# Kernel tuning notes

Hardware: AMD Instinct MI355X
Metric: run time of the kernel (lower is better)

## Reference

```python
import jax, jax.numpy as jnp
import numpy as np

B, N, K = 4, 16384, 8
NF = [8, 32, 64, 128, 256]
E = N * K


def setup_inputs() -> dict:
    key = jax.random.key(0)
    ks = jax.random.split(key, 16)
    x = jax.random.normal(ks[0], (B, N, NF[0]), jnp.float32)
    # knn-style edge list: every node appears as a center K times (no empty segments)
    centers = jnp.tile(jnp.repeat(jnp.arange(N), K)[None, None, :], (B, 1, 1))
    neighbors = jax.random.randint(ks[1], (B, 1, E), 0, N)
    edge_index = jnp.concatenate([centers, neighbors], axis=1)
    specs = [("0a", NF[0], NF[1]), ("0b", NF[0], NF[1]),
             ("1a", NF[1], NF[2]), ("1b", NF[1], NF[2]),
             ("2a", NF[2], NF[3]), ("2b", NF[2], NF[3]),
             ("3a", NF[3], NF[4]), ("3b", NF[3], NF[4]),
             ("cat", NF[1] + NF[2] + NF[3] + NF[4], 1)]
    inp = {"x": x, "edge_index": edge_index}
    for i, (nm, ci, co) in enumerate(specs):
        inp["W" + nm] = jax.random.normal(ks[2 + i], (ci, co), jnp.float32) / np.sqrt(ci)
        inp["g" + nm] = jnp.ones((co,), jnp.float32)   # BN gamma
        inp["b" + nm] = jnp.zeros((co,), jnp.float32)  # BN beta
    inp["bias"] = jnp.zeros((1,), jnp.float32)
    return inp


def _bn(x, g, b):
    # training-mode BatchNorm1d over all rows (GraphBatchNorm1d reduces over batch*num_points)
    m = x.mean(0)
    v = jnp.mean(jnp.square(x - m), 0)  # biased variance, as torch BN uses for normalization
    return g * (x - m) * jax.lax.rsqrt(v + 1e-5) + b


def _mlp(x, W, g, b):
    # Linear(bias=False) -> BN -> LeakyReLU(0.2)
    return jax.nn.leaky_relu(_bn(x @ W, g, b), negative_slope=0.2)


def reference(x, edge_index,
              W0a, g0a, b0a, W0b, g0b, b0b,
              W1a, g1a, b1a, W1b, g1b, b1b,
              W2a, g2a, b2a, W2b, g2b, b2b,
              W3a, g3a, b3a, W3b, g3b, b3b,
              Wcat, gcat, bcat, bias):
    BN = B * N
    xf = x.reshape(BN, NF[0])
    ei = edge_index.transpose(1, 0, 2).reshape(2, -1)  # [2, B*E]
    off = jnp.repeat(jnp.arange(B) * N, E)
    centers = ei[0] + off
    neighbors = ei[1] + off
    segmax = lambda v: jax.ops.segment_max(v, centers, num_segments=BN)
    x0 = _mlp(xf, W0a, g0a, b0a) + segmax(_mlp(xf[neighbors] - xf[centers], W0b, g0b, b0b))
    x1 = _mlp(x0, W1a, g1a, b1a) + segmax(_mlp(x0, W1b, g1b, b1b)[neighbors])
    x2 = _mlp(x1, W2a, g2a, b2a) + segmax(_mlp(x1, W2b, g2b, b2b)[neighbors])
    x3 = _mlp(x2, W3a, g3a, b3a) + segmax(_mlp(x2, W3b, g3b, b3b)[neighbors])
    x_cat = _mlp(jnp.concatenate([x0, x1, x2, x3], axis=-1), Wcat, gcat, bcat)
    return x_cat + bias
```

## Files before the change

kernel.cpp:

```cpp
#include <hip/hip_runtime.h>
#include <math.h>

static constexpr int BB = 4;
static constexpr int NN = 16384;
static constexpr int KK = 8;
static constexpr int EE = 131072;
static constexpr int RR = 65536;
static constexpr int EG = 524288;

static constexpr int SPL = 64;
static constexpr size_t SLOT = (size_t)SPL*512;

static constexpr size_t OFF_X0 = 0;
static constexpr size_t OFF_X1 = OFF_X0 + (size_t)RR*32;
static constexpr size_t OFF_X2 = OFF_X1 + (size_t)RR*64;
static constexpr size_t OFF_X3 = OFF_X2 + (size_t)RR*128;
static constexpr size_t OFF_ZB = OFF_X3 + (size_t)RR*256;
static constexpr size_t OFF_ZC = OFF_ZB + (size_t)RR*128;
static constexpr size_t OFF_S  = OFF_ZC + (size_t)RR;
static constexpr size_t OFF_WP = OFF_S + 9*SLOT;
static constexpr size_t OFF_MX = OFF_WP + 65536;
static constexpr size_t WP1_OFF = 0;
static constexpr size_t WP2_OFF = 4096;
static constexpr size_t WP3_OFF = 4096 + 16384;

__device__ __forceinline__ float lrelu(float x) { return fmaxf(x, 0.2f*x); }

__device__ __forceinline__ unsigned short f2h(float f) {
    _Float16 h = (_Float16)f;
    return *(unsigned short*)&h;
}
__device__ __forceinline__ float h2f(unsigned short u) {
    _Float16 h = *(_Float16*)&u;
    return (float)h;
}

typedef __attribute__((ext_vector_type(8))) _Float16 half8v;
typedef __attribute__((ext_vector_type(8))) unsigned short ushort8v;
typedef __attribute__((ext_vector_type(4))) float float4v;

__device__ __forceinline__ half8v h8max(half8v a, half8v b) {
#if __has_builtin(__builtin_elementwise_max)
    return __builtin_elementwise_max(a, b);
#else
    half8v r;
#pragma unroll
    for (int j = 0; j < 8; ++j) r[j] = (a[j] > b[j]) ? a[j] : b[j];
    return r;
#endif
}

__global__ __launch_bounds__(256) void k_l0_fused(const float* __restrict__ xf,
                                                  const int* __restrict__ ei,
                                                  const float* __restrict__ Wa,
                                                  const float* __restrict__ Wb,
                                                  const float* __restrict__ gb,
                                                  unsigned short* __restrict__ xa,
                                                  float* __restrict__ mxb,
                                                  float* __restrict__ Sa,
                                                  float* __restrict__ Sb) {
    __shared__ float wa[256], wb[256];
    __shared__ float red[128];
    __shared__ float sgns[32];
    int tid = threadIdx.x;
    wa[tid] = Wa[tid];
    wb[tid] = Wb[tid];
    if (tid < 128) red[tid] = 0.f;
    if (tid < 32) sgns[tid] = (gb[tid] >= 0.f) ? 1.f : -1.f;
    __syncthreads();
    int g = tid & 3, cg = g*8;
    int r = (blockIdx.x*256 + tid) >> 2;
    int b = r >> 14, n = r & (NN-1);
    const int4* nb4 = (const int4*)(ei + (size_t)b*2*EE + EE + n*KK);
    int4 q0v = nb4[0], q1v = nb4[1];
    int nbr[KK] = {q0v.x,q0v.y,q0v.z,q0v.w,q1v.x,q1v.y,q1v.z,q1v.w};
    const float4* pc = (const float4*)(xf + (size_t)r*8);
    float4 c0 = pc[0], c1 = pc[1];
    float xv[8] = {c0.x,c0.y,c0.z,c0.w,c1.x,c1.y,c1.z,c1.w};
    float sgn[8];
#pragma unroll
    for (int j = 0; j < 8; ++j) sgn[j] = sgns[cg+j];

    float4 nA[KK], nB[KK];
#pragma unroll
    for (int k = 0; k < KK; ++k) {
        const float4* pn = (const float4*)(xf + ((size_t)(b<<14) + nbr[k])*8);
        nA[k] = pn[0]; nB[k] = pn[1];
    }

    float opa[8];
#pragma unroll
    for (int j = 0; j < 8; ++j) {
        float s = 0.f;
#pragma unroll
        for (int k = 0; k < 8; ++k) s = fmaf(xv[k], wa[k*32+cg+j], s);
        opa[j] = s;
    }
    {
        ushort8v h;
#pragma unroll
        for (int j = 0; j < 8; ++j) h[j] = f2h(opa[j]);
        *(ushort8v*)&xa[(size_t)r*32 + cg] = h;
    }

    float s8[8], q8[8], mx[8];
#pragma unroll
    for (int j = 0; j < 8; ++j) { s8[j] = 0.f; q8[j] = 0.f; mx[j] = -3.0e38f; }
#pragma unroll
    for (int k = 0; k < KK; ++k) {
        float4 n0 = nA[k], n1 = nB[k];
        float d[8] = {n0.x-xv[0], n0.y-xv[1], n0.z-xv[2], n0.w-xv[3],
                      n1.x-xv[4], n1.y-xv[5], n1.z-xv[6], n1.w-xv[7]};
#pragma unroll
        for (int jj = 0; jj < 8; ++jj) {
            float z = 0.f;
#pragma unroll
            for (int k2 = 0; k2 < 8; ++k2) z = fmaf(d[k2], wb[k2*32+cg+jj], z);
            s8[jj] += z;
            q8[jj] = fmaf(z, z, q8[jj]);
            mx[jj] = fmaxf(mx[jj], sgn[jj]*z);
        }
    }
    {
        float4* mp = (float4*)&mxb[(size_t)r*32 + cg];
        mp[0] = (float4){mx[0],mx[1],mx[2],mx[3]};
        mp[1] = (float4){mx[4],mx[5],mx[6],mx[7]};
    }
    float sa8[8], qa8[8];
#pragma unroll
    for (int j = 0; j < 8; ++j) { sa8[j] = opa[j]; qa8[j] = opa[j]*opa[j]; }
#pragma unroll
    for (int off = 4; off <= 32; off <<= 1) {
#pragma unroll
        for (int j = 0; j < 8; ++j) {
            s8[j]  += __shfl_xor(s8[j],  off, 64);
            q8[j]  += __shfl_xor(q8[j],  off, 64);
            sa8[j] += __shfl_xor(sa8[j], off, 64);
            qa8[j] += __shfl_xor(qa8[j], off, 64);
        }
    }
    if ((tid & 63) < 4) {
#pragma unroll
        for (int j = 0; j < 8; ++j) {
            atomicAdd(&red[cg + j],       sa8[j]);
            atomicAdd(&red[32 + cg + j],  qa8[j]);
            atomicAdd(&red[64 + cg + j],  s8[j]);
            atomicAdd(&red[96 + cg + j],  q8[j]);
        }
    }
    __syncthreads();
    size_t pl = (size_t)(blockIdx.x & (SPL-1))*512;
    if (tid < 64) atomicAdd(&Sa[pl + tid], red[tid]);
    else if (tid < 128) atomicAdd(&Sb[pl + (tid - 64)], red[tid]);
}

__global__ __launch_bounds__(256) void k_edge_apply2(const float* __restrict__ mxb,
                                                     const float* __restrict__ Sa,
                                                     const float* __restrict__ Sb,
                                                     const float* __restrict__ ga,
                                                     const float* __restrict__ ba,
                                                     const float* __restrict__ gb,
                                                     const float* __restrict__ bbp,
                                                     const float* __restrict__ Wc,
                                                     unsigned short* __restrict__ x0,
                                                     float* __restrict__ zc) {
    __shared__ float scbA[32], shb[32], sca[32], sha[32], swc[32];
    int tid = threadIdx.x;
    if (tid < 32) {
        float su = 0.f, qu = 0.f;
        for (int p = 0; p < SPL; ++p) { su += Sa[(size_t)p*512 + tid]; qu += Sa[(size_t)p*512 + 32 + tid]; }
        float m = su*(1.f/RR);
        float v = fmaxf(qu*(1.f/RR) - m*m, 0.f);
        float sc = ga[tid]*rsqrtf(v + 1e-5f);
        sca[tid] = sc; sha[tid] = fmaf(-m, sc, ba[tid]);
        swc[tid] = Wc[tid];
    } else if (tid < 64) {
        int c = tid - 32;
        float su = 0.f, qu = 0.f;
        for (int p = 0; p < SPL; ++p) { su += Sb[(size_t)p*512 + c]; qu += Sb[(size_t)p*512 + 32 + c]; }
        float m = su*(1.f/EG);
        float v = fmaxf(qu*(1.f/EG) - m*m, 0.f);
        float sc = gb[c]*rsqrtf(v + 1e-5f);
        scbA[c] = fabsf(sc);
        shb[c] = fmaf(-m, sc, bbp[c]);
    }
    __syncthreads();
    int r = blockIdx.x*256 + tid;
    ushort8v* xp = (ushort8v*)(x0 + (size_t)r*32);
    const float4* mp = (const float4*)(mxb + (size_t)r*32);
    float sdot = 0.f;
#pragma unroll
    for (int i = 0; i < 4; ++i) {
        ushort8v v = xp[i];
        float4 m0 = mp[i*2], m1 = mp[i*2+1];
        float mx8[8] = {m0.x,m0.y,m0.z,m0.w,m1.x,m1.y,m1.z,m1.w};
        ushort8v o;
#pragma unroll
        for (int j = 0; j < 8; ++j) {
            int c = i*8 + j;
            float y = lrelu(fmaf(mx8[j], scbA[c], shb[c]));
            float val = lrelu(fmaf(h2f(v[j]), sca[c], sha[c])) + y;
            o[j] = f2h(val);
            sdot = fmaf(val, swc[c], sdot);
        }
        xp[i] = o;
    }
    zc[r] = sdot;
}

template<int CI, int CO>
__device__ __forceinline__ void packone(int t, const float* __restrict__ Wa,
                                        const float* __restrict__ Wb,
                                        unsigned short* __restrict__ Wp) {
    constexpr int NT = 2*CO;
    constexpr int KT = CI/32;
    int ng = t % NT, k = t / NT;
    float v = (ng < CO) ? Wa[(size_t)k*CO + ng] : Wb[(size_t)k*CO + (ng - CO)];
    int nt = ng >> 4, n = ng & 15;
    int kt = k >> 5, kq = (k & 31) >> 3, j = k & 7;
    int f = nt*KT + kt;
    int idx = f*512 + ((kq*16 + n)<<3) + j;
    Wp[idx] = f2h(v);
}

__global__ __launch_bounds__(256) void k_prep(const float* __restrict__ W1a, const float* __restrict__ W1b,
                                              const float* __restrict__ W2a, const float* __restrict__ W2b,
                                              const float* __restrict__ W3a, const float* __restrict__ W3b,
                                              unsigned short* __restrict__ wp1,
                                              unsigned short* __restrict__ wp2,
                                              unsigned short* __restrict__ wp3,
                                              float* __restrict__ S) {
    int t = blockIdx.x*256 + threadIdx.x;
    int NT_ = gridDim.x*256;
    for (int u = t; u < (int)(9*SLOT); u += NT_) S[u] = 0.f;
    for (int u = t; u < 32*128;  u += NT_) packone<32,64>(u, W1a, W1b, wp1);
    for (int u = t; u < 64*256;  u += NT_) packone<64,128>(u, W2a, W2b, wp2);
    for (int u = t; u < 128*512; u += NT_) packone<128,256>(u, W3a, W3b, wp3);
}

template<int CI, int CO, int MW>
__global__ __launch_bounds__(256, MW) void k_mfma_dual4(const unsigned short* __restrict__ X,
                                                        const unsigned short* __restrict__ Wp,
                                                        unsigned short* __restrict__ Za,
                                                        unsigned short* __restrict__ Zb,
                                                        float* __restrict__ Sa,
                                                        float* __restrict__ Sb) {
    constexpr int NCH = 4;
    constexpr int KT = CI/32;
    constexpr int WCNT = NCH*KT*512;
    constexpr int ROWT = RR/64;
    constexpr int STR = NCH*16 + 8;
    constexpr int XW  = (CI < 64) ? CI : 64;
    constexpr int PLB = CO/64;
    __shared__ unsigned short scr[4][16*STR];
    int tid = threadIdx.x;
    int lane = tid & 63, wid = tid >> 6;
    int ch = blockIdx.y;
    int wglob = blockIdx.x*4 + wid;
    int NW = gridDim.x*4;
    int n = lane & 15, kq = lane >> 4;
    int rg = lane >> 3, c8l = (lane & 7)*8;
    unsigned short* myscr = scr[wid];
    size_t pl = (size_t)(wglob & (SPL-1)) * 512;
    bool isA = (ch < PLB);
    unsigned short* Zp = (isA ? Za : Zb) + (size_t)(isA ? ch : ch - PLB)*((size_t)RR*64);

    half8v wreg[KT][NCH];
    {
        const unsigned short* Wc = Wp + (size_t)ch*WCNT;
#pragma unroll
        for (int kt = 0; kt < KT; ++kt)
#pragma unroll
            for (int j = 0; j < NCH; ++j)
                wreg[kt][j] = *(const half8v*)&Wc[(j*KT + kt)*512 + lane*8];
    }

    float4v ps[NCH], pq[NCH];
#pragma unroll
    for (int j = 0; j < NCH; ++j) { ps[j] = (float4v){0,0,0,0}; pq[j] = (float4v){0,0,0,0}; }

    auto issue = [&](half8v (&dst)[4], size_t rowb, int kt) {
        int k0 = kt*32 + kq*8;
        int xpl = k0 >> 6;
        int xoff = k0 & (XW-1);
        const unsigned short* Xp = X + (size_t)xpl*((size_t)RR*64);
#pragma unroll
        for (int i = 0; i < 4; ++i)
            dst[i] = *(const half8v*)&Xp[(rowb + i*16 + n)*XW + xoff];
    };

    auto domfma = [&](float4v (&acc)[4][NCH], half8v (&wk)[NCH], half8v (&bc)[4]) {
#pragma unroll
        for (int j = 0; j < NCH; ++j)
#pragma unroll
            for (int i = 0; i < 4; ++i)
                acc[i][j] = __builtin_amdgcn_mfma_f32_16x16x32_f16(wk[j], bc[i], acc[i][j], 0, 0, 0);
    };

    auto epilogue = [&](float4v (&acc)[4][NCH], size_t rowbase) {
#pragma unroll
        for (int j = 0; j < NCH; ++j)
#pragma unroll
            for (int i = 0; i < 4; ++i) {
                float4v a4 = acc[i][j];
#pragma unroll
                for (int reg = 0; reg < 4; ++reg) {
                    ps[j][reg] += a4[reg];
                    pq[j][reg] = fmaf(a4[reg], a4[reg], pq[j][reg]);
                }
            }
#pragma unroll
        for (int i = 0; i < 4; ++i) {
            __builtin_amdgcn_wave_barrier();
#pragma unroll
            for (int j = 0; j < NCH; ++j) {
                float4v a4 = acc[i][j];
                ushort4 h = { f2h(a4[0]), f2h(a4[1]), f2h(a4[2]), f2h(a4[3]) };
                *(ushort4*)&myscr[n*STR + j*16 + kq*4] = h;
            }
            __builtin_amdgcn_wave_barrier();
#pragma unroll
            for (int i2 = 0; i2 < 2; ++i2) {
                int rit = rg + i2*8;
                ushort8v v = *(const ushort8v*)&myscr[rit*STR + c8l];
                *(ushort8v*)&Zp[(rowbase + i*16 + rit)*64 + c8l] = v;
            }
        }
    };

    if constexpr (KT == 1) {
        half8v b0[4], b1[4];
        for (int t = wglob; t < ROWT; t += 2*NW) {
            int tB = t + NW;
            size_t rbA = (size_t)t*64;
            issue(b0, rbA, 0);
            bool hasB = (tB < ROWT);
            size_t rbB = hasB ? (size_t)tB*64 : rbA;
            if (hasB) issue(b1, rbB, 0);
            {
                float4v acc[4][NCH];
#pragma unroll
                for (int i = 0; i < 4; ++i)
#pragma unroll
                    for (int j = 0; j < NCH; ++j) acc[i][j] = (float4v){0,0,0,0};
                domfma(acc, wreg[0], b0);
                epilogue(acc, rbA);
            }
            if (hasB) {
                float4v acc[4][NCH];
#pragma unroll
                for (int i = 0; i < 4; ++i)
#pragma unroll
                    for (int j = 0; j < NCH; ++j) acc[i][j] = (float4v){0,0,0,0};
                domfma(acc, wreg[0], b1);
                epilogue(acc, rbB);
            }
        }
    } else if constexpr (KT == 4) {
        half8v p0[4], p1[4], p2[4], p3[4];
        int t = wglob;
        if (t < ROWT) {
            issue(p0, (size_t)t*64, 0);
            issue(p1, (size_t)t*64, 1);
        }
        for (; t < ROWT; t += NW) {
            size_t rowbase = (size_t)t*64;
            int t2 = t + NW;
            size_t nextrb = (t2 < ROWT) ? (size_t)t2*64 : rowbase;
            float4v acc[4][NCH];
#pragma unroll
            for (int i = 0; i < 4; ++i)
#pragma unroll
                for (int j = 0; j < NCH; ++j) acc[i][j] = (float4v){0,0,0,0};
            issue(p2, rowbase, 2);  domfma(acc, wreg[0], p0);
            issue(p3, rowbase, 3);  domfma(acc, wreg[1], p1);
            issue(p0, nextrb, 0);   domfma(acc, wreg[2], p2);
            issue(p1, nextrb, 1);   domfma(acc, wreg[3], p3);
            epilogue(acc, rowbase);
        }
    } else {
        half8v b0[4], b1[4];
        int t = wglob;
        if (t < ROWT) issue(b0, (size_t)t*64, 0);
        for (; t < ROWT; t += NW) {
            size_t rowbase = (size_t)t*64;
            int t2 = t + NW;
            size_t nextrb = (t2 < ROWT) ? (size_t)t2*64 : rowbase;
            float4v acc[4][NCH];
#pragma unroll
            for (int i = 0; i < 4; ++i)
#pragma unroll
                for (int j = 0; j < NCH; ++j) acc[i][j] = (float4v){0,0,0,0};
            issue(b1, rowbase, 1);  domfma(acc, wreg[0], b0);
            issue(b0, nextrb, 0);   domfma(acc, wreg[1], b1);
            epilogue(acc, rowbase);
        }
    }

    {
        float* Sg = isA ? Sa : Sb;
        int cb0 = isA ? ch*64 : ch*64 - CO;
#pragma unroll
        for (int j = 0; j < NCH; ++j) {
#pragma unroll
            for (int reg = 0; reg < 4; ++reg) {
                float s = ps[j][reg], q = pq[j][reg];
                s += __shfl_xor(s, 1, 64); q += __shfl_xor(q, 1, 64);
                s += __shfl_xor(s, 2, 64); q += __shfl_xor(q, 2, 64);
                s += __shfl_xor(s, 4, 64); q += __shfl_xor(q, 4, 64);
                s += __shfl_xor(s, 8, 64); q += __shfl_xor(q, 8, 64);
                if (n == 0) {
                    int col = cb0 + j*16 + kq*4 + reg;
                    atomicAdd(&Sg[pl + col], s);
                    atomicAdd(&Sg[pl + CO + col], q);
                }
            }
        }
    }
}

template<int CO>
__global__ __launch_bounds__(256) void k_redstats(float* __restrict__ Sa,
                                                  float* __restrict__ Sb) {
    int t = blockIdx.x*256 + threadIdx.x;
    for (int u = t; u < 2*CO; u += gridDim.x*256) {
        float sa = 0.f, sb = 0.f;
        for (int p = 1; p < SPL; ++p) {
            sa += Sa[(size_t)p*512 + u];
            sb += Sb[(size_t)p*512 + u];
        }
        Sa[u] += sa;
        Sb[u] += sb;
    }
}

template<int CO, bool WRITEBACK>
__global__ __launch_bounds__(256) void k_gathermax(unsigned short* __restrict__ xi,
                                                   const unsigned short* __restrict__ zbh,
                                                   const int* __restrict__ ei,
                                                   const float* __restrict__ Sa,
                                                   const float* __restrict__ Sb,
                                                   const float* __restrict__ ga,
                                                   const float* __restrict__ ba,
                                                   const float* __restrict__ gb,
                                                   const float* __restrict__ bbp,
                                                   const float* __restrict__ Wc,
                                                   int wcoff,
                                                   float* __restrict__ zc) {
    constexpr int CQ = CO/8;
    __shared__ float sca[CO], sha[CO], sbA[CO], shb[CO], swc[CO];
    __shared__ __attribute__((aligned(16))) unsigned short smk[CO];
    int tid = threadIdx.x;
    for (int u = tid; u < CO; u += 256) {
        float m = Sa[u]*(1.f/RR);
        float v = fmaxf(Sa[CO+u]*(1.f/RR) - m*m, 0.f);
        float sc = ga[u]*rsqrtf(v + 1e-5f);
        sca[u] = sc; sha[u] = fmaf(-m, sc, ba[u]);
        m = Sb[u]*(1.f/RR);
        v = fmaxf(Sb[CO+u]*(1.f/RR) - m*m, 0.f);
        sc = gb[u]*rsqrtf(v + 1e-5f);
        sbA[u] = fabsf(sc);
        smk[u] = (sc >= 0.f) ? (unsigned short)0 : (unsigned short)0x8000;
        shb[u] = fmaf(-m, sc, bbp[u]);
        swc[u] = Wc[wcoff + u];
    }
    __syncthreads();
    int bx = (int)((blockIdx.x & 7)*(gridDim.x >> 3) + (blockIdx.x >> 3));
    int t = bx*256 + tid;
    int r = t / CQ;
    int c8 = (t % CQ)*8;
    int pln = c8 >> 6;
    int off = c8 & 63;
    const unsigned short* zpl = zbh + (size_t)pln*((size_t)RR*64);
    unsigned short* xpl = xi + (size_t)pln*((size_t)RR*64);
    int b = r >> 14, n = r & (NN-1);
    const int4* nb4 = (const int4*)(ei + (size_t)b*2*EE + EE + n*KK);
    int4 q0 = nb4[0], q1 = nb4[1];
    int nbr[KK] = {q0.x,q0.y,q0.z,q0.w,q1.x,q1.y,q1.z,q1.w};
    size_t bb64 = ((size_t)(b<<14))*64 + off;
    ushort8v* xp = (ushort8v*)&xpl[(size_t)r*64 + off];
    ushort8v a = *xp;
    ushort8v u[KK];
#pragma unroll
    for (int k = 0; k < KK; ++k)
        u[k] = *(const ushort8v*)(zpl + bb64 + (size_t)nbr[k]*64);
    ushort8v msk8 = *(const ushort8v*)&smk[c8];
    ushort8v ninfu = {0xFC00,0xFC00,0xFC00,0xFC00,0xFC00,0xFC00,0xFC00,0xFC00};
    half8v mh = __builtin_bit_cast(half8v, ninfu);
#pragma unroll
    for (int k = 0; k < KK; ++k) {
        ushort8v uk = u[k] ^ msk8;
        mh = h8max(mh, __builtin_bit_cast(half8v, uk));
    }
    float sb[8], hb[8];
#pragma unroll
    for (int j = 0; j < 8; ++j) { sb[j] = sbA[c8+j]; hb[j] = shb[c8+j]; }
    float sdot = 0.f;
    if (WRITEBACK) {
        ushort8v o;
#pragma unroll
        for (int j = 0; j < 8; ++j) {
            int c = c8 + j;
            float y = lrelu(fmaf((float)mh[j], sb[j], hb[j]));
            float val = lrelu(fmaf(h2f(a[j]), sca[c], sha[c])) + y;
            o[j] = f2h(val);
            sdot = fmaf(val, swc[c], sdot);
        }
        *xp = o;
    } else {
#pragma unroll
        for (int j = 0; j < 8; ++j) {
            int c = c8 + j;
            float y = lrelu(fmaf((float)mh[j], sb[j], hb[j]));
            float val = lrelu(fmaf(h2f(a[j]), sca[c], sha[c])) + y;
            sdot = fmaf(val, swc[c], sdot);
        }
    }
#pragma unroll
    for (int w = CQ/2; w >= 1; w >>= 1) sdot += __shfl_xor(sdot, w, 64);
    int lane = tid & 63;
    if ((lane & (CQ-1)) == 0) atomicAdd(&zc[r], sdot);
}

__global__ __launch_bounds__(256) void k_catstats(const float* __restrict__ zc,
                                                  float* __restrict__ S8) {
    __shared__ float rs2[2];
    int tid = threadIdx.x;
    if (tid < 2) rs2[tid] = 0.f;
    __syncthreads();
    float v = zc[blockIdx.x*256 + tid];
    float s = v, q = v*v;
#pragma unroll
    for (int off = 32; off >= 1; off >>= 1) {
        s += __shfl_xor(s, off, 64);
        q += __shfl_xor(q, off, 64);
    }
    if ((tid & 63) == 0) { atomicAdd(&rs2[0], s); atomicAdd(&rs2[1], q); }
    __syncthreads();
    if (tid == 0) {
        int p = blockIdx.x & 255;
        atomicAdd(&S8[p*2],     rs2[0]);
        atomicAdd(&S8[p*2 + 1], rs2[1]);
    }
}

__global__ __launch_bounds__(256) void k_catfinal(const float* __restrict__ zc,
                                                  const float* __restrict__ S8,
                                                  const float* __restrict__ g,
                                                  const float* __restrict__ bb,
                                                  const float* __restrict__ bias,
                                                  float* __restrict__ out) {
    __shared__ float rs[256], rq[256];
    int tid = threadIdx.x;
    rs[tid] = S8[tid*2];
    rq[tid] = S8[tid*2 + 1];
    __syncthreads();
#pragma unroll
    for (int h = 128; h >= 1; h >>= 1) {
        if (tid < h) { rs[tid] += rs[tid+h]; rq[tid] += rq[tid+h]; }
        __syncthreads();
    }
    int r = blockIdx.x*256 + tid;
    const float invR = 1.f/65536.f;
    float m = rs[0]*invR;
    float v = fmaxf(rq[0]*invR - m*m, 0.f);
    float sc = g[0]*rsqrtf(v + 1e-5f);
    float sh = fmaf(-m, sc, bb[0]);
    float y = lrelu(fmaf(zc[r], sc, sh));
    out[r] = y + bias[0];
}

extern "C" void kernel_launch(void* const* d_in, const int* in_sizes, int n_in,
                              void* d_out, int out_size, void* d_ws, size_t ws_size,
                              hipStream_t stream) {
    const float* x    = (const float*)d_in[0];
    const int*   ei   = (const int*)d_in[1];
    const float* W0a  = (const float*)d_in[2];
    const float* g0a  = (const float*)d_in[3];
    const float* b0a  = (const float*)d_in[4];
    const float* W0b  = (const float*)d_in[5];
    const float* g0b  = (const float*)d_in[6];
    const float* b0b  = (const float*)d_in[7];
    const float* W1a  = (const float*)d_in[8];
    const float* g1a  = (const float*)d_in[9];
    const float* b1a  = (const float*)d_in[10];
    const float* W1b  = (const float*)d_in[11];
    const float* g1b  = (const float*)d_in[12];
    const float* b1b  = (const float*)d_in[13];
    const float* W2a  = (const float*)d_in[14];
    const float* g2a  = (const float*)d_in[15];
    const float* b2a  = (const float*)d_in[16];
    const float* W2b  = (const float*)d_in[17];
    const float* g2b  = (const float*)d_in[18];
    const float* b2b  = (const float*)d_in[19];
    const float* W3a  = (const float*)d_in[20];
    const float* g3a  = (const float*)d_in[21];
    const float* b3a  = (const float*)d_in[22];
    const float* W3b  = (const float*)d_in[23];
    const float* g3b  = (const float*)d_in[24];
    const float* b3b  = (const float*)d_in[25];
    const float* Wcat = (const float*)d_in[26];
    const float* gcat = (const float*)d_in[27];
    const float* bcat = (const float*)d_in[28];
    const float* bias = (const float*)d_in[29];
    float* out = (float*)d_out;

    float* ws = (float*)d_ws;
    unsigned short* x0 = (unsigned short*)(ws + OFF_X0);
    unsigned short* x1 = (unsigned short*)(ws + OFF_X1);
    unsigned short* x2 = (unsigned short*)(ws + OFF_X2);
    unsigned short* x3 = (unsigned short*)(ws + OFF_X3);
    unsigned short* zbh = (unsigned short*)(ws + OFF_ZB);
    float* zc = ws + OFF_ZC;
    float* S  = ws + OFF_S;
    unsigned short* wpbase = (unsigned short*)(ws + OFF_WP);
    unsigned short* wp1 = wpbase + WP1_OFF;
    unsigned short* wp2 = wpbase + WP2_OFF;
    unsigned short* wp3 = wpbase + WP3_OFF;
    float* mxb = ws + OFF_MX;
    auto Sl = [&](int i) { return S + (size_t)i*SLOT; };

    k_prep<<<256, 256, 0, stream>>>(W1a, W1b, W2a, W2b, W3a, W3b, wp1, wp2, wp3, S);

    k_l0_fused<<<RR*4/256, 256, 0, stream>>>(x, ei, W0a, W0b, g0b, x0, mxb, Sl(0), Sl(1));
    k_edge_apply2<<<RR/256, 256, 0, stream>>>(mxb, Sl(0), Sl(1),
                                              g0a, b0a, g0b, b0b, Wcat, x0, zc);

    k_mfma_dual4<32,64,3><<<dim3(128,2), 256, 0, stream>>>(x0, wp1, x1, zbh, Sl(2), Sl(3));
    k_redstats<64><<<4, 256, 0, stream>>>(Sl(2), Sl(3));
    k_gathermax<64,true><<<RR*8/256, 256, 0, stream>>>(x1, zbh, ei, Sl(2), Sl(3),
                                                       g1a, b1a, g1b, b1b, Wcat, 32, zc);

    k_mfma_dual4<64,128,3><<<dim3(128,4), 256, 0, stream>>>(x1, wp2, x2, zbh, Sl(4), Sl(5));
    k_redstats<128><<<4, 256, 0, stream>>>(Sl(4), Sl(5));
    k_gathermax<128,true><<<RR*16/256, 256, 0, stream>>>(x2, zbh, ei, Sl(4), Sl(5),
                                                         g2a, b2a, g2b, b2b, Wcat, 96, zc);

    k_mfma_dual4<128,256,2><<<dim3(64,8), 256, 0, stream>>>(x2, wp3, x3, zbh, Sl(6), Sl(7));
    k_redstats<256><<<4, 256, 0, stream>>>(Sl(6), Sl(7));
    k_gathermax<256,false><<<RR*32/256, 256, 0, stream>>>(x3, zbh, ei, Sl(6), Sl(7),
                                                          g3a, b3a, g3b, b3b, Wcat, 224, zc);

    k_catstats<<<RR/256, 256, 0, stream>>>(zc, Sl(8));
    k_catfinal<<<RR/256, 256, 0, stream>>>(zc, Sl(8), gcat, bcat, bias, out);
}
```

Baseline: 276.8 us.

## Fuse BN stat reduction into MFMA tail and remap gathermax blocks per XCD

```diff
diff --git a/kernel.cpp b/kernel.cpp
--- a/kernel.cpp
+++ b/kernel.cpp
@@ -23,6 +23,7 @@
 static constexpr size_t WP1_OFF = 0;
 static constexpr size_t WP2_OFF = 4096;
 static constexpr size_t WP3_OFF = 4096 + 16384;
+static constexpr size_t OFF_CTR = OFF_S + 8*SLOT + 2048;
 
 __device__ __forceinline__ float lrelu(float x) { return fmaxf(x, 0.2f*x); }
 
@@ -244,7 +245,8 @@
                                                         unsigned short* __restrict__ Za,
                                                         unsigned short* __restrict__ Zb,
                                                         float* __restrict__ Sa,
-                                                        float* __restrict__ Sb) {
+                                                        float* __restrict__ Sb,
+                                                        unsigned* __restrict__ ctr) {
     constexpr int NCH = 4;
     constexpr int KT = CI/32;
     constexpr int WCNT = NCH*KT*512;
@@ -253,6 +255,7 @@
     constexpr int XW  = (CI < 64) ? CI : 64;
     constexpr int PLB = CO/64;
     __shared__ unsigned short scr[4][16*STR];
+    __shared__ bool amLast;
     int tid = threadIdx.x;
     int lane = tid & 63, wid = tid >> 6;
     int ch = blockIdx.y;
@@ -417,20 +420,23 @@
             }
         }
     }
-}
-
-template<int CO>
-__global__ __launch_bounds__(256) void k_redstats(float* __restrict__ Sa,
-                                                  float* __restrict__ Sb) {
-    int t = blockIdx.x*256 + threadIdx.x;
-    for (int u = t; u < 2*CO; u += gridDim.x*256) {
-        float sa = 0.f, sb = 0.f;
-        for (int p = 1; p < SPL; ++p) {
-            sa += Sa[(size_t)p*512 + u];
-            sb += Sb[(size_t)p*512 + u];
-        }
-        Sa[u] += sa;
-        Sb[u] += sb;
+
+    __threadfence();
+    if (tid == 0) {
+        unsigned old = atomicAdd(ctr, 1u);
+        amLast = (old == (unsigned)(gridDim.x*gridDim.y) - 1u);
+    }
+    __syncthreads();
+    if (amLast) {
+        for (int u = tid; u < 2*CO; u += 256) {
+            float sa = 0.f, sb = 0.f;
+            for (int p = 0; p < SPL; ++p) {
+                sa += __hip_atomic_load(&Sa[(size_t)p*512 + u], __ATOMIC_RELAXED, __HIP_MEMORY_SCOPE_AGENT);
+                sb += __hip_atomic_load(&Sb[(size_t)p*512 + u], __ATOMIC_RELAXED, __HIP_MEMORY_SCOPE_AGENT);
+            }
+            Sa[u] = sa;
+            Sb[u] = sb;
+        }
     }
 }
 
@@ -447,7 +453,7 @@
                                                    const float* __restrict__ Wc,
                                                    int wcoff,
                                                    float* __restrict__ zc) {
-    constexpr int CQ = CO/8;
+    constexpr int P = CO/64;
     __shared__ float sca[CO], sha[CO], sbA[CO], shb[CO], swc[CO];
     __shared__ __attribute__((aligned(16))) unsigned short smk[CO];
     int tid = threadIdx.x;
@@ -465,15 +471,30 @@
         swc[u] = Wc[wcoff + u];
     }
     __syncthreads();
-    int bx = (int)((blockIdx.x & 7)*(gridDim.x >> 3) + (blockIdx.x >> 3));
-    int t = bx*256 + tid;
-    int r = t / CQ;
-    int c8 = (t % CQ)*8;
-    int pln = c8 >> 6;
-    int off = c8 & 63;
+    int bx = blockIdx.x;
+    int xcd = bx & 7;
+    int idx = bx >> 3;
+    int combo, inner;
+    if constexpr (P == 4) {
+        combo = xcd*2 + (idx >> 9);
+        inner = idx & 511;
+    } else if constexpr (P == 2) {
+        combo = xcd;
+        inner = idx;
+    } else {
+        combo = xcd >> 1;
+        inner = (idx << 1) | (xcd & 1);
+    }
+    int pln = combo >> 2;
+    int b   = combo & 3;
+    int t = inner*256 + tid;
+    int n = t >> 3;
+    int sub = t & 7;
+    int c8 = pln*64 + sub*8;
+    int off = sub*8;
+    int r = (b << 14) | n;
     const unsigned short* zpl = zbh + (size_t)pln*((size_t)RR*64);
     unsigned short* xpl = xi + (size_t)pln*((size_t)RR*64);
-    int b = r >> 14, n = r & (NN-1);
     const int4* nb4 = (const int4*)(ei + (size_t)b*2*EE + EE + n*KK);
     int4 q0 = nb4[0], q1 = nb4[1];
     int nbr[KK] = {q0.x,q0.y,q0.z,q0.w,q1.x,q1.y,q1.z,q1.w};
@@ -516,10 +537,10 @@
             sdot = fmaf(val, swc[c], sdot);
         }
     }
-#pragma unroll
-    for (int w = CQ/2; w >= 1; w >>= 1) sdot += __shfl_xor(sdot, w, 64);
-    int lane = tid & 63;
-    if ((lane & (CQ-1)) == 0) atomicAdd(&zc[r], sdot);
+    sdot += __shfl_xor(sdot, 1, 64);
+    sdot += __shfl_xor(sdot, 2, 64);
+    sdot += __shfl_xor(sdot, 4, 64);
+    if (sub == 0) atomicAdd(&zc[r], sdot);
 }
 
 __global__ __launch_bounds__(256) void k_catstats(const float* __restrict__ zc,
@@ -618,6 +639,7 @@
     unsigned short* wp2 = wpbase + WP2_OFF;
     unsigned short* wp3 = wpbase + WP3_OFF;
     float* mxb = ws + OFF_MX;
+    unsigned* ctrs = (unsigned*)(ws + OFF_CTR);
     auto Sl = [&](int i) { return S + (size_t)i*SLOT; };
 
     k_prep<<<256, 256, 0, stream>>>(W1a, W1b, W2a, W2b, W3a, W3b, wp1, wp2, wp3, S);
@@ -626,18 +648,15 @@
     k_edge_apply2<<<RR/256, 256, 0, stream>>>(mxb, Sl(0), Sl(1),
                                               g0a, b0a, g0b, b0b, Wcat, x0, zc);
 
-    k_mfma_dual4<32,64,3><<<dim3(128,2), 256, 0, stream>>>(x0, wp1, x1, zbh, Sl(2), Sl(3));
-    k_redstats<64><<<4, 256, 0, stream>>>(Sl(2), Sl(3));
+    k_mfma_dual4<32,64,3><<<dim3(128,2), 256, 0, stream>>>(x0, wp1, x1, zbh, Sl(2), Sl(3), ctrs + 0);
     k_gathermax<64,true><<<RR*8/256, 256, 0, stream>>>(x1, zbh, ei, Sl(2), Sl(3),
                                                        g1a, b1a, g1b, b1b, Wcat, 32, zc);
 
-    k_mfma_dual4<64,128,3><<<dim3(128,4), 256, 0, stream>>>(x1, wp2, x2, zbh, Sl(4), Sl(5));
-    k_redstats<128><<<4, 256, 0, stream>>>(Sl(4), Sl(5));
+    k_mfma_dual4<64,128,3><<<dim3(128,4), 256, 0, stream>>>(x1, wp2, x2, zbh, Sl(4), Sl(5), ctrs + 1);
     k_gathermax<128,true><<<RR*16/256, 256, 0, stream>>>(x2, zbh, ei, Sl(4), Sl(5),
                                                          g2a, b2a, g2b, b2b, Wcat, 96, zc);
 
-    k_mfma_dual4<128,256,2><<<dim3(64,8), 256, 0, stream>>>(x2, wp3, x3, zbh, Sl(6), Sl(7));
-    k_redstats<256><<<4, 256, 0, stream>>>(Sl(6), Sl(7));
+    k_mfma_dual4<128,256,2><<<dim3(64,8), 256, 0, stream>>>(x2, wp3, x3, zbh, Sl(6), Sl(7), ctrs + 2);
     k_gathermax<256,false><<<RR*32/256, 256, 0, stream>>>(x3, zbh, ei, Sl(6), Sl(7),
                                                           g3a, b3a, g3b, b3b, Wcat, 224, zc);
 
```

Result: slower. 350.8 us (+26.7%).
